# Optimization experiments

Hardware: AMD Instinct MI355X
Metric: run time of the kernel (lower is better)

## Reference

```python
import jax, jax.numpy as jnp
import numpy as np

GROUPS = 32
EPS = 1e-5


def group_norm(x, scale, bias):
    # x: [b, v, t, s, f]; normalize per (b,v,t) sample over (channels_in_group, s)
    b, v, t, s, f = x.shape
    xg = x.reshape(b, v, t, s, GROUPS, f // GROUPS)
    mean = xg.mean(axis=(3, 5), keepdims=True)
    var = xg.var(axis=(3, 5), keepdims=True)
    xn = ((xg - mean) * jax.lax.rsqrt(var + EPS)).reshape(b, v, t, s, f)
    return xn * scale + bias


def nh_conv(x, adjc, W, b):
    # x: [b,v,t,s,f_in]; adjc: [s, k]; W: [k, f_in, f_out]; b: [f_out]
    x_nh = x[:, :, :, adjc, :]                      # [b,v,t,s,k,f_in]
    return jnp.einsum('bvtskf,kfo->bvtso', x_nh, W) + b


def setup_inputs() -> dict:
    key = jax.random.key(0)
    ks = jax.random.split(key, 12)
    B, V, T, S, F_IN, F_OUT, K = 1, 2, 2, 12288, 128, 256, 9
    x = jax.random.normal(ks[0], (B, V, T, S, F_IN), dtype=jnp.float32)
    adjc = jax.random.randint(ks[1], (S, K), 0, S, dtype=jnp.int32)
    gn1_scale = jnp.ones((F_IN,), jnp.float32)
    gn1_bias = jnp.zeros((F_IN,), jnp.float32)
    gn2_scale = jnp.ones((F_OUT,), jnp.float32)
    gn2_bias = jnp.zeros((F_OUT,), jnp.float32)
    W_skip = jax.random.normal(ks[2], (F_IN, F_OUT), jnp.float32) / np.sqrt(F_IN)
    b_skip = jnp.zeros((F_OUT,), jnp.float32)
    W1 = jax.random.normal(ks[3], (K, F_IN, F_OUT), jnp.float32) / np.sqrt(K * F_IN)
    b1 = jnp.zeros((F_OUT,), jnp.float32)
    W2 = jax.random.normal(ks[4], (K, F_OUT, F_OUT), jnp.float32) / np.sqrt(K * F_OUT)
    b2 = jnp.zeros((F_OUT,), jnp.float32)
    return dict(x=x, adjc=adjc, gn1_scale=gn1_scale, gn1_bias=gn1_bias,
                gn2_scale=gn2_scale, gn2_bias=gn2_bias, W_skip=W_skip, b_skip=b_skip,
                W1=W1, b1=b1, W2=W2, b2=b2)


def reference(x, gn1_scale, gn1_bias, gn2_scale, gn2_bias, W_skip, b_skip,
              W1, b1, W2, b2, adjc):
    # skip_layer: ProjLayer with zoom_diff=0 -> plain Linear in->out
    x_res = jnp.einsum('bvtsf,fo->bvtso', x, W_skip) + b_skip
    # norm1 + SiLU (updownconv is Identity when zooms match and in==in feats)
    h = jax.nn.silu(group_norm(x, gn1_scale, gn1_bias))
    # conv1: neighbor-gather linear [k, f_in] -> f_out
    h = nh_conv(h, adjc, W1, b1)
    # emb_layer = Identity; norm2 + SiLU
    h = jax.nn.silu(group_norm(h, gn2_scale, gn2_bias))
    # conv2 + residual
    h = nh_conv(h, adjc, W2, b2)
    return h + x_res
```

## Files before the change

### kernel.cpp

```cpp
#include <hip/hip_runtime.h>
#include <hip/hip_bf16.h>

typedef __bf16 bf16_t;
typedef __bf16 bf16x8 __attribute__((ext_vector_type(8)));
typedef float f32x4 __attribute__((ext_vector_type(4)));

#define S_TOT 12288
#define F_IN 128
#define F_OUT 256
#define EPS 1e-5f

static __device__ __forceinline__ float silu_f(float v) {
  return v / (1.0f + __expf(-v));
}

static __device__ __forceinline__ void gll16(const bf16_t* g, bf16_t* l) {
  __builtin_amdgcn_global_load_lds(
      (const __attribute__((address_space(1))) void*)(const void*)g,
      (__attribute__((address_space(3))) void*)(void*)l, 16, 0, 0);
}

__global__ void pack_weights(const float* __restrict__ W1,
                             const float* __restrict__ W2,
                             const float* __restrict__ Wsk,
                             bf16_t* __restrict__ W1p,
                             bf16_t* __restrict__ W2p,
                             bf16_t* __restrict__ Wsp) {
  int w = blockIdx.x * 4 + (threadIdx.x >> 6);
  int l = threadIdx.x & 63;
  int lo = l & 15, hi = l >> 4;
  const float* src;
  bf16_t* dst;
  int fbase, obase;
  if (w < 576) {
    int k = w >> 6, rem = w & 63, kc = rem >> 4, cb = rem & 15;
    src = W1 + k * 32768;
    dst = W1p + (size_t)w * 512;
    fbase = 32 * kc + 8 * hi; obase = 16 * cb + lo;
  } else if (w < 1728) {
    int idx = w - 576;
    int k = idx >> 7, rem = idx & 127, kc = rem >> 4, cb = rem & 15;
    src = W2 + k * 65536;
    dst = W2p + (size_t)idx * 512;
    fbase = 32 * kc + 8 * hi; obase = 16 * cb + lo;
  } else {
    int idx = w - 1728;
    int kc = idx >> 4, cb = idx & 15;
    src = Wsk;
    dst = Wsp + (size_t)idx * 512;
    fbase = 32 * kc + 8 * hi; obase = 16 * cb + lo;
  }
  bf16x8 v;
#pragma unroll
  for (int j = 0; j < 8; ++j)
    v[j] = (bf16_t)src[(fbase + j) * 256 + obase];
  *(bf16x8*)(dst + l * 8) = v;
}

__global__ void gn1_stats(const float* __restrict__ x,
                          float* __restrict__ sum1, float* __restrict__ ss1) {
  int vt = blockIdx.y;
  int s0 = blockIdx.x * 256;
  int t = threadIdx.x;
  int col = t & 31, ro = t >> 5;
  float s_ = 0.f, q_ = 0.f;
  const f32x4* xp = (const f32x4*)(x + ((size_t)vt * S_TOT + s0) * F_IN);
#pragma unroll 4
  for (int it = 0; it < 32; ++it) {
    f32x4 v = xp[(size_t)(it * 8 + ro) * 32 + col];
    s_ += v[0] + v[1] + v[2] + v[3];
    q_ += v[0]*v[0] + v[1]*v[1] + v[2]*v[2] + v[3]*v[3];
  }
  __shared__ float gs[32], gq[32];
  if (t < 32) { gs[t] = 0.f; gq[t] = 0.f; }
  __syncthreads();
  atomicAdd(&gs[col], s_);
  atomicAdd(&gq[col], q_);
  __syncthreads();
  if (t < 32) {
    atomicAdd(&sum1[vt * 32 + t], gs[t]);
    atomicAdd(&ss1[vt * 32 + t], gq[t]);
  }
}

__global__ void apply_gn1(const float* __restrict__ x,
                          const float* __restrict__ sum1, const float* __restrict__ ss1,
                          const float* __restrict__ gs, const float* __restrict__ gb,
                          bf16_t* __restrict__ h1) {
  size_t base = ((size_t)blockIdx.x * 256 + threadIdx.x) * 8;
  int vt = (int)(base / ((size_t)S_TOT * F_IN));
  int c0 = (int)(base & (F_IN - 1));
  const f32x4* xp = (const f32x4*)(x + base);
  f32x4 v0 = xp[0], v1 = xp[1];
  float N = (float)(S_TOT * 4);
  bf16x8 o;
#pragma unroll
  for (int gi = 0; gi < 2; ++gi) {
    int g = (c0 >> 2) + gi;
    float mean = sum1[vt * 32 + g] / N;
    float var = ss1[vt * 32 + g] / N - mean * mean;
    float r = rsqrtf(var + EPS);
    f32x4 v = gi ? v1 : v0;
#pragma unroll
    for (int j = 0; j < 4; ++j) {
      int c = g * 4 + j;
      float a = r * gs[c];
      float b = gb[c] - mean * a;
      o[gi * 4 + j] = (bf16_t)silu_f(v[j] * a + b);
    }
  }
  *(bf16x8*)(h1 + base) = o;
}

__global__ void apply_gn2(bf16_t* __restrict__ h,
                          const float* __restrict__ sum_c, const float* __restrict__ ss_c,
                          const float* __restrict__ gs, const float* __restrict__ gb) {
  size_t base = ((size_t)blockIdx.x * 256 + threadIdx.x) * 8;
  int vt = (int)(base / ((size_t)S_TOT * F_OUT));
  int c0 = (int)(base & (F_OUT - 1));
  int g = c0 >> 3;
  bf16x8 v = *(const bf16x8*)(h + base);
  float sg = 0.f, qg = 0.f;
#pragma unroll
  for (int j = 0; j < 8; ++j) {
    sg += sum_c[vt * 256 + g * 8 + j];
    qg += ss_c[vt * 256 + g * 8 + j];
  }
  float N = (float)(S_TOT * 8);
  float mean = sg / N;
  float var = qg / N - mean * mean;
  float r = rsqrtf(var + EPS);
  bf16x8 o;
#pragma unroll
  for (int j = 0; j < 8; ++j) {
    int c = g * 8 + j;
    float a = r * gs[c];
    float b = gb[c] - mean * a;
    o[j] = (bf16_t)silu_f((float)v[j] * a + b);
  }
  *(bf16x8*)(h + base) = o;
}

template<int RE, int NSUB, bool XSK>
__global__ __launch_bounds__(256, 3) void conv_kernel(
    const bf16_t* __restrict__ hsrc, const bf16_t* __restrict__ Wp,
    const bf16_t* __restrict__ Wsp, const float* __restrict__ x,
    const int* __restrict__ adjc, const float* __restrict__ bias,
    const float* __restrict__ biask, bf16_t* __restrict__ outb,
    float* __restrict__ outf, float* __restrict__ sum_c, float* __restrict__ ss_c) {
  const int tid = threadIdx.x;
  const int wv = tid >> 6, l = tid & 63;
  const int lo = l & 15, hi = l >> 4;
  const int mw = wv >> 1, nw = wv & 1;

  int swz = ((blockIdx.x & 7) * 96) + (blockIdx.x >> 3);
  int vt = swz / 192;
  int rem = swz - vt * 192;
  int sblk = rem >> 1, nsp = rem & 1;
  int s0 = sblk * 128;

  __shared__ int adjs[1152];
  __shared__ bf16_t ab[3][4096];
  __shared__ bf16_t bb[3][4096];

  for (int i = tid; i < 1152; i += 256) adjs[i] = adjc[s0 * 9 + i];
  __syncthreads();

  const bf16_t* hb = hsrc + (size_t)vt * ((size_t)S_TOT * RE);
  constexpr int TPK = RE / 32;
  constexpr int NMAIN = XSK ? (NSUB - 4) : NSUB;

  auto stageA = [&](int buf, int s) {
    int tap = s / TPK, chunk = s % TPK;
#pragma unroll
    for (int j2 = 0; j2 < 2; ++j2) {
      int j = wv * 2 + j2;
      int row = j * 16 + (l >> 2);
      int segs = (l & 3) ^ ((row >> 1) & 3);
      int arow = adjs[row * 9 + tap];
      const bf16_t* g = hb + (size_t)arow * RE + chunk * 32 + segs * 8;
      gll16(g, &ab[buf][j * 512]);
    }
  };
  auto stageB = [&](int buf, const bf16_t* wsrc, int kcg) {
#pragma unroll
    for (int j2 = 0; j2 < 2; ++j2) {
      int ul = wv * 2 + j2;
      const bf16_t* g = wsrc + ((size_t)(kcg * 16 + nsp * 8 + ul)) * 512 + l * 8;
      gll16(g, &bb[buf][ul * 512]);
    }
  };
  auto stageX = [&](int buf, int sx) {
    int row = tid >> 1, h = tid & 1;
    const float* xr = x + ((size_t)vt * S_TOT + s0 + row) * F_IN + sx * 32 + h * 16;
    f32x4 xv[4];
#pragma unroll
    for (int i = 0; i < 4; ++i) xv[i] = *(const f32x4*)(xr + i * 4);
#pragma unroll
    for (int i = 0; i < 2; ++i) {
      bf16x8 w;
#pragma unroll
      for (int jj = 0; jj < 4; ++jj) {
        w[jj] = (bf16_t)xv[2 * i][jj];
        w[4 + jj] = (bf16_t)xv[2 * i + 1][jj];
      }
      int seg = 2 * h + i;
      *(bf16x8*)(&ab[buf][row * 32 + (((seg ^ ((row >> 1) & 3))) << 3)]) = w;
    }
  };

  f32x4 acc[4][4] = {};
  auto compute = [&](int buf) {
    bf16x8 bfr[4];
#pragma unroll
    for (int ni = 0; ni < 4; ++ni)
      bfr[ni] = *(const bf16x8*)(&bb[buf][(nw * 4 + ni) * 512 + l * 8]);
    bf16x8 afr[4];
#pragma unroll
    for (int mi = 0; mi < 4; ++mi) {
      int rr = mw * 64 + mi * 16 + lo;
      afr[mi] = *(const bf16x8*)(&ab[buf][rr * 32 + ((hi ^ ((rr >> 1) & 3)) << 3)]);
    }
    __builtin_amdgcn_s_setprio(1);
#pragma unroll
    for (int mi = 0; mi < 4; ++mi)
#pragma unroll
      for (int ni = 0; ni < 4; ++ni)
        acc[mi][ni] = __builtin_amdgcn_mfma_f32_16x16x32_bf16(afr[mi], bfr[ni], acc[mi][ni], 0, 0, 0);
    __builtin_amdgcn_s_setprio(0);
  };

  stageA(0, 0); stageB(0, Wp, 0);
  stageA(1, 1); stageB(1, Wp, 1);
  for (int s = 0; s < NMAIN; ++s) {
    if (s + 1 < NMAIN) asm volatile("s_waitcnt vmcnt(4)" ::: "memory");
    else               asm volatile("s_waitcnt vmcnt(0)" ::: "memory");
    __builtin_amdgcn_s_barrier();
    __builtin_amdgcn_sched_barrier(0);
    int s2 = s + 2;
    if (s2 < NMAIN) {
      int nb = s2 % 3;
      stageA(nb, s2);
      stageB(nb, Wp, s2);
    }
    compute(s % 3);
  }

  if (XSK) {
    for (int sx = 0; sx < 4; ++sx) {
      int cur = (NMAIN + sx) % 3;
      __syncthreads();
      stageX(cur, sx);
      stageB(cur, Wsp, sx);
      __syncthreads();
      compute(cur);
    }
  }

  if (!XSK) {
    bf16_t* ob = outb + ((size_t)vt * S_TOT + s0) * 256;
#pragma unroll
    for (int ni = 0; ni < 4; ++ni) {
      int o = nsp * 128 + nw * 64 + ni * 16 + lo;
      float bv = bias[o];
      float s_ = 0.f, q_ = 0.f;
#pragma unroll
      for (int mi = 0; mi < 4; ++mi)
#pragma unroll
        for (int r2 = 0; r2 < 4; ++r2) {
          int srow = mw * 64 + mi * 16 + hi * 4 + r2;
          float v = acc[mi][ni][r2] + bv;
          ob[(size_t)srow * 256 + o] = (bf16_t)v;
          s_ += v; q_ += v * v;
        }
      s_ += __shfl_xor(s_, 16); s_ += __shfl_xor(s_, 32);
      q_ += __shfl_xor(q_, 16); q_ += __shfl_xor(q_, 32);
      if (hi == 0) {
        atomicAdd(&sum_c[vt * 256 + o], s_);
        atomicAdd(&ss_c[vt * 256 + o], q_);
      }
    }
  } else {
    float* of = outf + ((size_t)vt * S_TOT + s0) * 256;
#pragma unroll
    for (int ni = 0; ni < 4; ++ni) {
      int o = nsp * 128 + nw * 64 + ni * 16 + lo;
      float bv = bias[o] + biask[o];
#pragma unroll
      for (int mi = 0; mi < 4; ++mi)
#pragma unroll
        for (int r2 = 0; r2 < 4; ++r2) {
          int srow = mw * 64 + mi * 16 + hi * 4 + r2;
          of[(size_t)srow * 256 + o] = acc[mi][ni][r2] + bv;
        }
    }
  }
}

extern "C" void kernel_launch(void* const* d_in, const int* in_sizes, int n_in,
                              void* d_out, int out_size, void* d_ws, size_t ws_size,
                              hipStream_t stream) {
  const float* x      = (const float*)d_in[0];
  const int*   adjc   = (const int*)d_in[1];
  const float* gn1_s  = (const float*)d_in[2];
  const float* gn1_b  = (const float*)d_in[3];
  const float* gn2_s  = (const float*)d_in[4];
  const float* gn2_b  = (const float*)d_in[5];
  const float* W_skip = (const float*)d_in[6];
  const float* b_skip = (const float*)d_in[7];
  const float* W1     = (const float*)d_in[8];
  const float* b1     = (const float*)d_in[9];
  const float* W2     = (const float*)d_in[10];
  const float* b2     = (const float*)d_in[11];
  float* out = (float*)d_out;

  float* sum1  = (float*)d_ws;
  float* ss1   = sum1 + 128;
  float* sum_c = ss1 + 128;
  float* ss_c  = sum_c + 1024;
  float* pad   = ss_c + 1024;
  bf16_t* W1p  = (bf16_t*)(pad + 3072);
  bf16_t* W2p  = W1p + 294912;
  bf16_t* Wsp  = W2p + 589824;
  bf16_t* h1   = Wsp + 32768;
  bf16_t* out1 = h1 + 6291456;

  hipMemsetAsync(sum1, 0, (128 + 128 + 1024 + 1024) * sizeof(float), stream);
  pack_weights<<<448, 256, 0, stream>>>(W1, W2, W_skip, W1p, W2p, Wsp);
  gn1_stats<<<dim3(48, 4), 256, 0, stream>>>(x, sum1, ss1);
  apply_gn1<<<3072, 256, 0, stream>>>(x, sum1, ss1, gn1_s, gn1_b, h1);
  conv_kernel<128, 36, false><<<768, 256, 0, stream>>>(
      h1, W1p, nullptr, nullptr, adjc, b1, nullptr, out1, nullptr, sum_c, ss_c);
  apply_gn2<<<6144, 256, 0, stream>>>(out1, sum_c, ss_c, gn2_s, gn2_b);
  conv_kernel<256, 76, true><<<768, 256, 0, stream>>>(
      out1, W2p, Wsp, x, adjc, b2, b_skip, nullptr, out, nullptr, nullptr);
}
```

Measured before the change: 153.2 us.

## Retile conv to 96x256 blocks with weights loaded directly into registers

Each conv block now covers 96 rows and all 256 output columns, and each wave owns 64 columns, so the grid drops from 768 to 512 blocks. The gathered activations are no longer read twice by two column-split blocks. Weights are loaded with inline-asm global loads straight into registers, double-buffered, which removes the LDS weight buffers. The main loop is unrolled by two with hand-placed waitcnts. Waves 2-3 issue dummy weight loads into unused LDS slots to keep vmcnt counts uniform. The weight-pack and GN1-stats kernels are merged into one launch, and launch bounds drop to 2 blocks per SM, trading occupancy for larger accumulators.

```diff
diff --git a/kernel.cpp b/kernel.cpp
--- a/kernel.cpp
+++ b/kernel.cpp
@@ -4,6 +4,7 @@
 typedef __bf16 bf16_t;
 typedef __bf16 bf16x8 __attribute__((ext_vector_type(8)));
 typedef float f32x4 __attribute__((ext_vector_type(4)));
+typedef int i32x4 __attribute__((ext_vector_type(4)));
 
 #define S_TOT 12288
 #define F_IN 128
@@ -20,66 +21,68 @@
       (__attribute__((address_space(3))) void*)(void*)l, 16, 0, 0);
 }
 
-__global__ void pack_weights(const float* __restrict__ W1,
-                             const float* __restrict__ W2,
-                             const float* __restrict__ Wsk,
-                             bf16_t* __restrict__ W1p,
-                             bf16_t* __restrict__ W2p,
-                             bf16_t* __restrict__ Wsp) {
-  int w = blockIdx.x * 4 + (threadIdx.x >> 6);
-  int l = threadIdx.x & 63;
-  int lo = l & 15, hi = l >> 4;
-  const float* src;
-  bf16_t* dst;
-  int fbase, obase;
-  if (w < 576) {
-    int k = w >> 6, rem = w & 63, kc = rem >> 4, cb = rem & 15;
-    src = W1 + k * 32768;
-    dst = W1p + (size_t)w * 512;
-    fbase = 32 * kc + 8 * hi; obase = 16 * cb + lo;
-  } else if (w < 1728) {
-    int idx = w - 576;
-    int k = idx >> 7, rem = idx & 127, kc = rem >> 4, cb = rem & 15;
-    src = W2 + k * 65536;
-    dst = W2p + (size_t)idx * 512;
-    fbase = 32 * kc + 8 * hi; obase = 16 * cb + lo;
+__global__ void prep_kernel(const float* __restrict__ W1,
+                            const float* __restrict__ W2,
+                            const float* __restrict__ Wsk,
+                            bf16_t* __restrict__ W1p,
+                            bf16_t* __restrict__ W2p,
+                            bf16_t* __restrict__ Wsp,
+                            const float* __restrict__ x,
+                            float* __restrict__ sum1, float* __restrict__ ss1) {
+  __shared__ float gs[32], gq[32];
+  if (blockIdx.x < 448) {
+    int w = blockIdx.x * 4 + (threadIdx.x >> 6);
+    int l = threadIdx.x & 63;
+    int lo = l & 15, hi = l >> 4;
+    const float* src;
+    bf16_t* dst;
+    int fbase, obase;
+    if (w < 576) {
+      int k = w >> 6, rem = w & 63, kc = rem >> 4, cb = rem & 15;
+      src = W1 + k * 32768;
+      dst = W1p + (size_t)w * 512;
+      fbase = 32 * kc + 8 * hi; obase = 16 * cb + lo;
+    } else if (w < 1728) {
+      int idx = w - 576;
+      int k = idx >> 7, rem = idx & 127, kc = rem >> 4, cb = rem & 15;
+      src = W2 + k * 65536;
+      dst = W2p + (size_t)idx * 512;
+      fbase = 32 * kc + 8 * hi; obase = 16 * cb + lo;
+    } else {
+      int idx = w - 1728;
+      int kc = idx >> 4, cb = idx & 15;
+      src = Wsk;
+      dst = Wsp + (size_t)idx * 512;
+      fbase = 32 * kc + 8 * hi; obase = 16 * cb + lo;
+    }
+    bf16x8 v;
+#pragma unroll
+    for (int j = 0; j < 8; ++j)
+      v[j] = (bf16_t)src[(fbase + j) * 256 + obase];
+    *(bf16x8*)(dst + l * 8) = v;
   } else {
-    int idx = w - 1728;
-    int kc = idx >> 4, cb = idx & 15;
-    src = Wsk;
-    dst = Wsp + (size_t)idx * 512;
-    fbase = 32 * kc + 8 * hi; obase = 16 * cb + lo;
-  }
-  bf16x8 v;
-#pragma unroll
-  for (int j = 0; j < 8; ++j)
-    v[j] = (bf16_t)src[(fbase + j) * 256 + obase];
-  *(bf16x8*)(dst + l * 8) = v;
-}
-
-__global__ void gn1_stats(const float* __restrict__ x,
-                          float* __restrict__ sum1, float* __restrict__ ss1) {
-  int vt = blockIdx.y;
-  int s0 = blockIdx.x * 256;
-  int t = threadIdx.x;
-  int col = t & 31, ro = t >> 5;
-  float s_ = 0.f, q_ = 0.f;
-  const f32x4* xp = (const f32x4*)(x + ((size_t)vt * S_TOT + s0) * F_IN);
+    int blk = blockIdx.x - 448;
+    int vt = blk & 3;
+    int s0 = (blk >> 2) * 256;
+    int t = threadIdx.x;
+    int col = t & 31, ro = t >> 5;
+    float s_ = 0.f, q_ = 0.f;
+    const f32x4* xp = (const f32x4*)(x + ((size_t)vt * S_TOT + s0) * F_IN);
 #pragma unroll 4
-  for (int it = 0; it < 32; ++it) {
-    f32x4 v = xp[(size_t)(it * 8 + ro) * 32 + col];
-    s_ += v[0] + v[1] + v[2] + v[3];
-    q_ += v[0]*v[0] + v[1]*v[1] + v[2]*v[2] + v[3]*v[3];
-  }
-  __shared__ float gs[32], gq[32];
-  if (t < 32) { gs[t] = 0.f; gq[t] = 0.f; }
-  __syncthreads();
-  atomicAdd(&gs[col], s_);
-  atomicAdd(&gq[col], q_);
-  __syncthreads();
-  if (t < 32) {
-    atomicAdd(&sum1[vt * 32 + t], gs[t]);
-    atomicAdd(&ss1[vt * 32 + t], gq[t]);
+    for (int it = 0; it < 32; ++it) {
+      f32x4 v = xp[(size_t)(it * 8 + ro) * 32 + col];
+      s_ += v[0] + v[1] + v[2] + v[3];
+      q_ += v[0]*v[0] + v[1]*v[1] + v[2]*v[2] + v[3]*v[3];
+    }
+    if (t < 32) { gs[t] = 0.f; gq[t] = 0.f; }
+    __syncthreads();
+    atomicAdd(&gs[col], s_);
+    atomicAdd(&gq[col], q_);
+    __syncthreads();
+    if (t < 32) {
+      atomicAdd(&sum1[vt * 32 + t], gs[t]);
+      atomicAdd(&ss1[vt * 32 + t], gq[t]);
+    }
   }
 }
 
@@ -142,7 +145,7 @@
 }
 
 template<int RE, int NSUB, bool XSK>
-__global__ __launch_bounds__(256, 3) void conv_kernel(
+__global__ __launch_bounds__(256, 2) void conv_kernel(
     const bf16_t* __restrict__ hsrc, const bf16_t* __restrict__ Wp,
     const bf16_t* __restrict__ Wsp, const float* __restrict__ x,
     const int* __restrict__ adjc, const float* __restrict__ bias,
@@ -151,19 +154,17 @@
   const int tid = threadIdx.x;
   const int wv = tid >> 6, l = tid & 63;
   const int lo = l & 15, hi = l >> 4;
-  const int mw = wv >> 1, nw = wv & 1;
-
-  int swz = ((blockIdx.x & 7) * 96) + (blockIdx.x >> 3);
-  int vt = swz / 192;
-  int rem = swz - vt * 192;
-  int sblk = rem >> 1, nsp = rem & 1;
-  int s0 = sblk * 128;
-
-  __shared__ int adjs[1152];
+  const int nw = wv;
+
+  int swz = ((blockIdx.x & 7) << 6) + (blockIdx.x >> 3);
+  int vt = swz >> 7;
+  int sblk = swz & 127;
+  int s0 = sblk * 96;
+
+  __shared__ int adjs[864];
   __shared__ bf16_t ab[3][4096];
-  __shared__ bf16_t bb[3][4096];
-
-  for (int i = tid; i < 1152; i += 256) adjs[i] = adjc[s0 * 9 + i];
+
+  for (int i = tid; i < 864; i += 256) adjs[i] = adjc[s0 * 9 + i];
   __syncthreads();
 
   const bf16_t* hb = hsrc + (size_t)vt * ((size_t)S_TOT * RE);
@@ -171,89 +172,129 @@
   constexpr int NMAIN = XSK ? (NSUB - 4) : NSUB;
 
   auto stageA = [&](int buf, int s) {
-    int tap = s / TPK, chunk = s % TPK;
-#pragma unroll
-    for (int j2 = 0; j2 < 2; ++j2) {
-      int j = wv * 2 + j2;
+    int tap = s / TPK, chunk = s - tap * TPK;
+    {
+      int j = wv;
       int row = j * 16 + (l >> 2);
       int segs = (l & 3) ^ ((row >> 1) & 3);
-      int arow = adjs[row * 9 + tap];
-      const bf16_t* g = hb + (size_t)arow * RE + chunk * 32 + segs * 8;
+      const bf16_t* g = hb + (size_t)adjs[row * 9 + tap] * RE + chunk * 32 + segs * 8;
       gll16(g, &ab[buf][j * 512]);
     }
+    if (wv < 2) {
+      int j = 4 + wv;
+      int row = j * 16 + (l >> 2);
+      int segs = (l & 3) ^ ((row >> 1) & 3);
+      const bf16_t* g = hb + (size_t)adjs[row * 9 + tap] * RE + chunk * 32 + segs * 8;
+      gll16(g, &ab[buf][j * 512]);
+    } else {
+      gll16(Wp + l * 8, &ab[buf][(4 + wv) * 512]);
+    }
   };
-  auto stageB = [&](int buf, const bf16_t* wsrc, int kcg) {
-#pragma unroll
-    for (int j2 = 0; j2 < 2; ++j2) {
-      int ul = wv * 2 + j2;
-      const bf16_t* g = wsrc + ((size_t)(kcg * 16 + nsp * 8 + ul)) * 512 + l * 8;
-      gll16(g, &bb[buf][ul * 512]);
-    }
+
+  auto asmB = [&](i32x4* dst, const bf16_t* wsrc, int kcg) {
+    const bf16_t* p = wsrc + (size_t)kcg * 8192 + nw * 2048 + l * 8;
+    asm volatile(
+        "global_load_dwordx4 %0, %4, off\n\t"
+        "global_load_dwordx4 %1, %4, off offset:1024\n\t"
+        "global_load_dwordx4 %2, %4, off offset:2048\n\t"
+        "global_load_dwordx4 %3, %4, off offset:3072"
+        : "=&v"(dst[0]), "=&v"(dst[1]), "=&v"(dst[2]), "=&v"(dst[3])
+        : "v"(p));
   };
+
   auto stageX = [&](int buf, int sx) {
-    int row = tid >> 1, h = tid & 1;
-    const float* xr = x + ((size_t)vt * S_TOT + s0 + row) * F_IN + sx * 32 + h * 16;
-    f32x4 xv[4];
-#pragma unroll
-    for (int i = 0; i < 4; ++i) xv[i] = *(const f32x4*)(xr + i * 4);
-#pragma unroll
-    for (int i = 0; i < 2; ++i) {
-      bf16x8 w;
-#pragma unroll
-      for (int jj = 0; jj < 4; ++jj) {
-        w[jj] = (bf16_t)xv[2 * i][jj];
-        w[4 + jj] = (bf16_t)xv[2 * i + 1][jj];
+    if (tid < 192) {
+      int row = tid >> 1, h = tid & 1;
+      const float* xr = x + ((size_t)vt * S_TOT + s0 + row) * F_IN + sx * 32 + h * 16;
+      f32x4 xv[4];
+#pragma unroll
+      for (int i = 0; i < 4; ++i) xv[i] = *(const f32x4*)(xr + i * 4);
+#pragma unroll
+      for (int i = 0; i < 2; ++i) {
+        bf16x8 w;
+#pragma unroll
+        for (int jj = 0; jj < 4; ++jj) {
+          w[jj] = (bf16_t)xv[2 * i][jj];
+          w[4 + jj] = (bf16_t)xv[2 * i + 1][jj];
+        }
+        int seg = 2 * h + i;
+        *(bf16x8*)(&ab[buf][row * 32 + ((seg ^ ((row >> 1) & 3)) << 3)]) = w;
       }
-      int seg = 2 * h + i;
-      *(bf16x8*)(&ab[buf][row * 32 + (((seg ^ ((row >> 1) & 3))) << 3)]) = w;
     }
   };
 
-  f32x4 acc[4][4] = {};
-  auto compute = [&](int buf) {
-    bf16x8 bfr[4];
-#pragma unroll
-    for (int ni = 0; ni < 4; ++ni)
-      bfr[ni] = *(const bf16x8*)(&bb[buf][(nw * 4 + ni) * 512 + l * 8]);
-    bf16x8 afr[4];
-#pragma unroll
-    for (int mi = 0; mi < 4; ++mi) {
-      int rr = mw * 64 + mi * 16 + lo;
+  f32x4 acc[6][4] = {};
+  auto compute = [&](int buf, const i32x4* bv) {
+    bf16x8 afr[6];
+#pragma unroll
+    for (int mi = 0; mi < 6; ++mi) {
+      int rr = mi * 16 + lo;
       afr[mi] = *(const bf16x8*)(&ab[buf][rr * 32 + ((hi ^ ((rr >> 1) & 3)) << 3)]);
     }
     __builtin_amdgcn_s_setprio(1);
 #pragma unroll
-    for (int mi = 0; mi < 4; ++mi)
+    for (int mi = 0; mi < 6; ++mi)
 #pragma unroll
       for (int ni = 0; ni < 4; ++ni)
-        acc[mi][ni] = __builtin_amdgcn_mfma_f32_16x16x32_bf16(afr[mi], bfr[ni], acc[mi][ni], 0, 0, 0);
+        acc[mi][ni] = __builtin_amdgcn_mfma_f32_16x16x32_bf16(
+            afr[mi], __builtin_bit_cast(bf16x8, bv[ni]), acc[mi][ni], 0, 0, 0);
     __builtin_amdgcn_s_setprio(0);
   };
 
-  stageA(0, 0); stageB(0, Wp, 0);
-  stageA(1, 1); stageB(1, Wp, 1);
-  for (int s = 0; s < NMAIN; ++s) {
-    if (s + 1 < NMAIN) asm volatile("s_waitcnt vmcnt(4)" ::: "memory");
-    else               asm volatile("s_waitcnt vmcnt(0)" ::: "memory");
+  i32x4 b0[4], b1[4];
+  stageA(0, 0);
+  stageA(1, 1);
+  asmB(b0, Wp, 0);
+  int bcur3 = 0, bstg3 = 2;
+
+  for (int s = 0; s < NMAIN - 2; s += 2) {
+    asm volatile("s_waitcnt vmcnt(6)" ::: "memory");
     __builtin_amdgcn_s_barrier();
     __builtin_amdgcn_sched_barrier(0);
-    int s2 = s + 2;
-    if (s2 < NMAIN) {
-      int nb = s2 % 3;
-      stageA(nb, s2);
-      stageB(nb, Wp, s2);
-    }
-    compute(s % 3);
-  }
+    stageA(bstg3, s + 2);
+    asmB(b1, Wp, s + 1);
+    asm volatile("s_waitcnt vmcnt(6)" ::: "memory");
+    __builtin_amdgcn_sched_barrier(0);
+    compute(bcur3, b0);
+    bcur3 = (bcur3 == 2) ? 0 : bcur3 + 1;
+    bstg3 = (bstg3 == 2) ? 0 : bstg3 + 1;
+    asm volatile("s_waitcnt vmcnt(6)" ::: "memory");
+    __builtin_amdgcn_s_barrier();
+    __builtin_amdgcn_sched_barrier(0);
+    stageA(bstg3, s + 3);
+    asmB(b0, Wp, s + 2);
+    asm volatile("s_waitcnt vmcnt(6)" ::: "memory");
+    __builtin_amdgcn_sched_barrier(0);
+    compute(bcur3, b1);
+    bcur3 = (bcur3 == 2) ? 0 : bcur3 + 1;
+    bstg3 = (bstg3 == 2) ? 0 : bstg3 + 1;
+  }
+  asm volatile("s_waitcnt vmcnt(6)" ::: "memory");
+  __builtin_amdgcn_s_barrier();
+  __builtin_amdgcn_sched_barrier(0);
+  asmB(b1, Wp, NMAIN - 1);
+  asm volatile("s_waitcnt vmcnt(4)" ::: "memory");
+  __builtin_amdgcn_sched_barrier(0);
+  compute(bcur3, b0);
+  bcur3 = (bcur3 == 2) ? 0 : bcur3 + 1;
+  asm volatile("s_waitcnt vmcnt(4)" ::: "memory");
+  __builtin_amdgcn_s_barrier();
+  __builtin_amdgcn_sched_barrier(0);
+  asm volatile("s_waitcnt vmcnt(0)" ::: "memory");
+  __builtin_amdgcn_sched_barrier(0);
+  compute(bcur3, b1);
 
   if (XSK) {
+#pragma unroll
     for (int sx = 0; sx < 4; ++sx) {
-      int cur = (NMAIN + sx) % 3;
+      int tb = sx & 1;
       __syncthreads();
-      stageX(cur, sx);
-      stageB(cur, Wsp, sx);
+      stageX(tb, sx);
+      if (sx & 1) asmB(b1, Wsp, sx); else asmB(b0, Wsp, sx);
+      asm volatile("s_waitcnt vmcnt(0)" ::: "memory");
       __syncthreads();
-      compute(cur);
+      __builtin_amdgcn_sched_barrier(0);
+      compute(tb, (sx & 1) ? (const i32x4*)b1 : (const i32x4*)b0);
     }
   }
 
@@ -261,14 +302,14 @@
     bf16_t* ob = outb + ((size_t)vt * S_TOT + s0) * 256;
 #pragma unroll
     for (int ni = 0; ni < 4; ++ni) {
-      int o = nsp * 128 + nw * 64 + ni * 16 + lo;
+      int o = nw * 64 + ni * 16 + lo;
       float bv = bias[o];
       float s_ = 0.f, q_ = 0.f;
 #pragma unroll
-      for (int mi = 0; mi < 4; ++mi)
+      for (int mi = 0; mi < 6; ++mi)
 #pragma unroll
         for (int r2 = 0; r2 < 4; ++r2) {
-          int srow = mw * 64 + mi * 16 + hi * 4 + r2;
+          int srow = mi * 16 + hi * 4 + r2;
           float v = acc[mi][ni][r2] + bv;
           ob[(size_t)srow * 256 + o] = (bf16_t)v;
           s_ += v; q_ += v * v;
@@ -284,13 +325,13 @@
     float* of = outf + ((size_t)vt * S_TOT + s0) * 256;
 #pragma unroll
     for (int ni = 0; ni < 4; ++ni) {
-      int o = nsp * 128 + nw * 64 + ni * 16 + lo;
+      int o = nw * 64 + ni * 16 + lo;
       float bv = bias[o] + biask[o];
 #pragma unroll
-      for (int mi = 0; mi < 4; ++mi)
+      for (int mi = 0; mi < 6; ++mi)
 #pragma unroll
         for (int r2 = 0; r2 < 4; ++r2) {
-          int srow = mw * 64 + mi * 16 + hi * 4 + r2;
+          int srow = mi * 16 + hi * 4 + r2;
           of[(size_t)srow * 256 + o] = acc[mi][ni][r2] + bv;
         }
     }
@@ -326,12 +367,11 @@
   bf16_t* out1 = h1 + 6291456;
 
   hipMemsetAsync(sum1, 0, (128 + 128 + 1024 + 1024) * sizeof(float), stream);
-  pack_weights<<<448, 256, 0, stream>>>(W1, W2, W_skip, W1p, W2p, Wsp);
-  gn1_stats<<<dim3(48, 4), 256, 0, stream>>>(x, sum1, ss1);
+  prep_kernel<<<640, 256, 0, stream>>>(W1, W2, W_skip, W1p, W2p, Wsp, x, sum1, ss1);
   apply_gn1<<<3072, 256, 0, stream>>>(x, sum1, ss1, gn1_s, gn1_b, h1);
-  conv_kernel<128, 36, false><<<768, 256, 0, stream>>>(
+  conv_kernel<128, 36, false><<<512, 256, 0, stream>>>(
       h1, W1p, nullptr, nullptr, adjc, b1, nullptr, out1, nullptr, sum_c, ss_c);
   apply_gn2<<<6144, 256, 0, stream>>>(out1, sum_c, ss_c, gn2_s, gn2_b);
-  conv_kernel<256, 76, true><<<768, 256, 0, stream>>>(
+  conv_kernel<256, 76, true><<<512, 256, 0, stream>>>(
       out1, W2p, Wsp, x, adjc, b2, b_skip, nullptr, out, nullptr, nullptr);
 }
```

After: 152.2 us. About the same (-0.6%).
